# Kernel optimization log

Hardware: AMD Instinct MI355X
Metric: run time of the kernel (lower is better)

Reference implementation:

```python
import jax, jax.numpy as jnp
import numpy as np

H = 128
N_CAN = 100000
N_FLAG = 50000
E = 600000
L = 500000


def _sage_conv(x_src, x_dst, edge_index, Wl, bl, Wr):
    # PyG SAGEConv (mean aggr): lin_l(mean_{j in N(i)} x_j) + lin_r(x_i)
    src, dst = edge_index[0], edge_index[1]
    msg = x_src[src]                                        # [E, H] gather
    n_dst = x_dst.shape[0]
    agg = jax.ops.segment_sum(msg, dst, num_segments=n_dst)  # [N_dst, H]
    cnt = jax.ops.segment_sum(jnp.ones((msg.shape[0],), msg.dtype), dst,
                              num_segments=n_dst)
    mean = agg / jnp.maximum(cnt, 1.0)[:, None]
    return mean @ Wl.T + bl + x_dst @ Wr.T


def setup_inputs() -> dict:
    key = jax.random.key(0)
    ks = jax.random.split(key, 16)
    s = 1.0 / np.sqrt(H)
    inp = {
        'can_node_id': jnp.arange(N_CAN, dtype=jnp.int64) if jax.config.jax_enable_x64 else jnp.arange(N_CAN, dtype=jnp.int32),
        'flag_node_id': jnp.arange(N_FLAG, dtype=jnp.int32),
        'edge_index_cf': jnp.stack([
            jax.random.randint(ks[0], (E,), 0, N_CAN),
            jax.random.randint(ks[1], (E,), 0, N_FLAG)]),
        'edge_index_fc': jnp.stack([
            jax.random.randint(ks[2], (E,), 0, N_FLAG),
            jax.random.randint(ks[3], (E,), 0, N_CAN)]),
        'edge_label_index': jnp.stack([
            jax.random.randint(ks[4], (L,), 0, N_CAN),
            jax.random.randint(ks[5], (L,), 0, N_FLAG)]),
        'can_emb': jax.random.normal(ks[6], (N_CAN, H), jnp.float32),
        'flag_emb': jax.random.normal(ks[7], (N_FLAG, H), jnp.float32),
        # SAGEConv for edge type CAN->flag (updates flag nodes)
        'Wl_cf': jax.random.normal(ks[8], (H, H), jnp.float32) * s,
        'bl_cf': jnp.zeros((H,), jnp.float32),
        'Wr_cf': jax.random.normal(ks[9], (H, H), jnp.float32) * s,
        # SAGEConv for edge type flag->CAN (updates CAN nodes)
        'Wl_fc': jax.random.normal(ks[10], (H, H), jnp.float32) * s,
        'bl_fc': jnp.zeros((H,), jnp.float32),
        'Wr_fc': jax.random.normal(ks[11], (H, H), jnp.float32) * s,
        # classifier MLP
        'W1': jax.random.normal(ks[12], (H, 2 * H), jnp.float32) * (1.0 / np.sqrt(2 * H)),
        'b1': jnp.zeros((H,), jnp.float32),
        'W2': jax.random.normal(ks[13], (1, H), jnp.float32) * s,
        'b2': jnp.zeros((1,), jnp.float32),
    }
    return inp


def reference(can_node_id, flag_node_id, edge_index_cf, edge_index_fc,
              edge_label_index, can_emb, flag_emb,
              Wl_cf, bl_cf, Wr_cf, Wl_fc, bl_fc, Wr_fc,
              W1, b1, W2, b2):
    # embedding lookups
    x_can = can_emb[can_node_id]    # [N_CAN, H]
    x_flag = flag_emb[flag_node_id]  # [N_FLAG, H]
    # to_hetero single SAGE layer + relu (dropout is identity in eval)
    upd_flag = jax.nn.relu(_sage_conv(x_can, x_flag, edge_index_cf, Wl_cf, bl_cf, Wr_cf))
    upd_can = jax.nn.relu(_sage_conv(x_flag, x_can, edge_index_fc, Wl_fc, bl_fc, Wr_fc))
    # link prediction classifier
    src = upd_can[edge_label_index[0]]   # [L, H]
    dst = upd_flag[edge_label_index[1]]  # [L, H]
    h = jax.nn.relu(jnp.concatenate([src, dst], axis=-1) @ W1.T + b1)
    out = h @ W2.T + b2
    return out.reshape(-1)
```

## Files before the change

kernel.cpp:

```cpp
#include <hip/hip_runtime.h>
#include <hip/hip_bf16.h>

#define H 128
#define BSH 8
#define MAXB 1024
#define PCH 4096
#define PIT (PCH / 256)

typedef __attribute__((ext_vector_type(8))) short short8;
typedef __attribute__((ext_vector_type(4))) short short4v;
typedef __attribute__((ext_vector_type(4))) float floatx4;
typedef unsigned short ushort_t;
typedef unsigned int uint_t;

__device__ __forceinline__ short f2bf(float f) {
    __hip_bfloat16 h = __float2bfloat16(f);
    return *reinterpret_cast<short*>(&h);
}
__device__ __forceinline__ float bflo(uint_t u) { return __uint_as_float(u << 16); }
__device__ __forceinline__ float bfhi(uint_t u) { return __uint_as_float(u & 0xFFFF0000u); }
__device__ __forceinline__ uint_t pack_bf2(float x, float y) {
    return (uint_t)(ushort_t)f2bf(x) | ((uint_t)(ushort_t)f2bf(y) << 16);
}
__device__ __forceinline__ void acc8(float* acc, uint4 r) {
    acc[0] += bflo(r.x); acc[1] += bfhi(r.x);
    acc[2] += bflo(r.y); acc[3] += bfhi(r.y);
    acc[4] += bflo(r.z); acc[5] += bfhi(r.z);
    acc[6] += bflo(r.w); acc[7] += bfhi(r.w);
}

__global__ __launch_bounds__(256)
void bucket_hist_cvt_kernel(const int* __restrict__ ei1, const int* __restrict__ ei2,
                            int E, int NF, int B, int* __restrict__ bcnt, int nbh,
                            const float* __restrict__ a, int n4a,
                            const float* __restrict__ b, int n4b,
                            ushort_t* __restrict__ da, ushort_t* __restrict__ db,
                            const float* __restrict__ Wl_cf, const float* __restrict__ Wr_cf,
                            const float* __restrict__ Wl_fc, const float* __restrict__ Wr_fc,
                            const float* __restrict__ W1, ushort_t* __restrict__ wb) {
    __shared__ int h[MAXB];
    int tid = threadIdx.x;
    if ((int)blockIdx.x < nbh) {
        for (int i = tid; i < B; i += 256) h[i] = 0;
        __syncthreads();
        int base = blockIdx.x * PCH;
        #pragma unroll 4
        for (int it = 0; it < PIT; ++it) {
            int t = base + it * 256 + tid;
            if (t < 2 * E) {
                int g = (t < E) ? ei1[E + t] : (ei2[E + t - E] + NF);
                atomicAdd(&h[g >> BSH], 1);
            }
        }
        __syncthreads();
        for (int i = tid; i < B; i += 256)
            if (h[i]) atomicAdd(&bcnt[i], h[i]);
        return;
    }
    int i = ((int)blockIdx.x - nbh) * 256 + tid;
    const float* src; ushort_t* dst; int k;
    if (i < n4a) { src = a; dst = da; k = i; }
    else if (i < n4a + n4b) { src = b; dst = db; k = i - n4a; }
    else {
        int idx = (i - n4a - n4b) * 4;
        if (idx >= 98304) return;
        int off;
        if      (idx < 16384) { src = Wl_cf; off = idx; }
        else if (idx < 32768) { src = Wr_cf; off = idx - 16384; }
        else if (idx < 49152) { src = Wl_fc; off = idx - 32768; }
        else if (idx < 65536) { src = Wr_fc; off = idx - 49152; }
        else                  { src = W1;    off = idx - 65536; }
        float4 v = *(const float4*)(src + off);
        short4v s;
        s[0] = f2bf(v.x); s[1] = f2bf(v.y); s[2] = f2bf(v.z); s[3] = f2bf(v.w);
        *(short4v*)(wb + idx) = s;
        return;
    }
    float4 v = ((const float4*)src)[k];
    short4v s;
    s[0] = f2bf(v.x); s[1] = f2bf(v.y); s[2] = f2bf(v.z); s[3] = f2bf(v.w);
    ((short4v*)dst)[k] = s;
}

__global__ __launch_bounds__(256)
void partition_kernel(const int* __restrict__ ei1, const int* __restrict__ ei2,
                      int E, int NF, int B, const int* __restrict__ bcnt,
                      int* __restrict__ bfront, uint_t* __restrict__ part) {
    __shared__ int h[MAXB];
    __shared__ int basex[MAXB];
    __shared__ int sdata[256];
    int tid = threadIdx.x;
    {
        int base4 = tid * 4;
        int v[4]; int s = 0;
        #pragma unroll
        for (int i = 0; i < 4; ++i) { int idx = base4 + i; v[i] = (idx < B) ? bcnt[idx] : 0; s += v[i]; }
        sdata[tid] = s;
        __syncthreads();
        for (int off = 1; off < 256; off <<= 1) {
            int t = (tid >= off) ? sdata[tid - off] : 0;
            __syncthreads();
            sdata[tid] += t;
            __syncthreads();
        }
        int excl = tid ? sdata[tid - 1] : 0;
        #pragma unroll
        for (int i = 0; i < 4; ++i) {
            int idx = base4 + i;
            if (idx < B) basex[idx] = excl;
            excl += v[i];
        }
    }
    for (int i = tid; i < B; i += 256) h[i] = 0;
    __syncthreads();

    int base = blockIdx.x * PCH;
    int pay[PIT]; int bkv[PIT]; int rv[PIT];
    #pragma unroll
    for (int it = 0; it < PIT; ++it) {
        int t = base + it * 256 + tid;
        bkv[it] = -1;
        if (t < 2 * E) {
            int g, s;
            if (t < E) { g = ei1[E + t]; s = ei1[t]; }
            else       { int e = t - E; g = ei2[E + e] + NF; s = ei2[e]; }
            int bk = g >> BSH;
            bkv[it] = bk;
            rv[it] = atomicAdd(&h[bk], 1);
            pay[it] = (int)(((uint_t)(g & 255) << 24) | (uint_t)s);
        }
    }
    __syncthreads();
    for (int i = tid; i < B; i += 256) {
        int c = h[i];
        if (c) basex[i] += atomicAdd(&bfront[i], c);
    }
    __syncthreads();
    #pragma unroll
    for (int it = 0; it < PIT; ++it) {
        if (bkv[it] >= 0)
            part[basex[bkv[it]] + rv[it]] = (uint_t)pay[it];
    }
}

__global__ __launch_bounds__(256)
void fine_bin_kernel(const int* __restrict__ bcnt, int B, int nTot, int E2,
                     const uint_t* __restrict__ part,
                     int* __restrict__ offs, int* __restrict__ bins) {
    __shared__ int cnt[256];
    __shared__ int sdata[256];
    __shared__ int excl[256];
    int b = blockIdx.x;
    int tid = threadIdx.x;
    {
        int partial = 0;
        for (int i = tid; i < b; i += 256) partial += bcnt[i];
        sdata[tid] = partial;
        __syncthreads();
        for (int off = 128; off > 0; off >>= 1) {
            if (tid < off) sdata[tid] += sdata[tid + off];
            __syncthreads();
        }
    }
    int seg0 = sdata[0];
    int seg1 = seg0 + bcnt[b];
    int gbase = b << BSH;
    __syncthreads();
    cnt[tid] = 0;
    __syncthreads();
    for (int k = seg0 + tid; k < seg1; k += 256)
        atomicAdd(&cnt[part[k] >> 24], 1);
    __syncthreads();
    sdata[tid] = cnt[tid];
    __syncthreads();
    for (int off = 1; off < 256; off <<= 1) {
        int t = (tid >= off) ? sdata[tid - off] : 0;
        __syncthreads();
        sdata[tid] += t;
        __syncthreads();
    }
    excl[tid] = tid ? sdata[tid - 1] : 0;
    int g = gbase + tid;
    if (g < nTot) offs[g] = seg0 + excl[tid];
    if (b == 0 && tid == 0) offs[nTot] = E2;
    cnt[tid] = 0;
    __syncthreads();
    for (int k = seg0 + tid; k < seg1; k += 256) {
        uint_t e = part[k];
        int l = (int)(e >> 24);
        int r = atomicAdd(&cnt[l], 1);
        bins[seg0 + excl[l] + r] = (int)(e & 0x00FFFFFFu);
    }
}

__global__ __launch_bounds__(256)
void sage4_kernel(int nbF, int NF, int NC,
                  const int* __restrict__ offs, const int* __restrict__ bins,
                  ushort_t* __restrict__ outf, const ushort_t* __restrict__ embf,
                  ushort_t* __restrict__ outc, const ushort_t* __restrict__ embc,
                  const ushort_t* __restrict__ wlf, const ushort_t* __restrict__ wrf,
                  const float* __restrict__ blf,
                  const ushort_t* __restrict__ wlc, const ushort_t* __restrict__ wrc,
                  const float* __restrict__ blc,
                  const ushort_t* __restrict__ W1) {
    __shared__ short A[64][136];
    bool isF = (int)blockIdx.x < nbF;
    int nrows = isF ? NF : NC;
    int rbase = (isF ? blockIdx.x : blockIdx.x - nbF) * 64;
    ushort_t* io = isF ? outf : outc;
    const ushort_t* embS = isF ? embf : embc;
    const ushort_t* embN = isF ? embc : embf;
    const ushort_t* Wl = isF ? wlf : wlc;
    const ushort_t* Wr = isF ? wrf : wrc;
    const float* bl = isF ? blf : blc;
    int koff = isF ? 128 : 0;
    int gofs = isF ? 0 : NF;

    int tid = threadIdx.x;
    int lane = tid & 63;
    int wv = tid >> 6;
    int l15 = lane & 15;
    int quad = lane >> 4;
    int nb0 = 32 * wv + l15;

    float blv0 = bl[nb0];
    float blv1 = bl[nb0 + 16];

    {
        const ushort_t* epN = embN + l15 * 8;
        #pragma unroll
        for (int half = 0; half < 2; ++half) {
            int r0 = wv * 16 + half * 8 + quad;
            int r1 = r0 + 4;
            int row0 = rbase + r0, row1 = rbase + r1;
            int st0 = 0, en0 = 0, st1 = 0, en1 = 0;
            if (row0 < nrows) { int g = gofs + row0; st0 = offs[g]; en0 = offs[g + 1]; }
            if (row1 < nrows) { int g = gofs + row1; st1 = offs[g]; en1 = offs[g + 1]; }
            int d0 = en0 - st0, d1 = en1 - st1;
            int n0 = d0 < 16 ? d0 : 16;
            int n1 = d1 < 16 ? d1 : 16;
            int pre0 = (l15 < n0) ? bins[st0 + l15] : 0;
            int pre1 = (l15 < n1) ? bins[st1 + l15] : 0;

            float a0[8], a1[8];
            #pragma unroll
            for (int t = 0; t < 8; ++t) { a0[t] = 0.f; a1[t] = 0.f; }

            int nmax = n0 > n1 ? n0 : n1;
            for (int k = 0; k < nmax; k += 2) {
                int s00 = __shfl(pre0, k,     16);
                int s01 = __shfl(pre0, k + 1, 16);
                int s10 = __shfl(pre1, k,     16);
                int s11 = __shfl(pre1, k + 1, 16);
                bool b00 = k < n0, b01 = (k + 1) < n0;
                bool b10 = k < n1, b11 = (k + 1) < n1;
                uint4 q00, q01, q10, q11;
                if (b00) q00 = *(const uint4*)(epN + (size_t)s00 * H);
                if (b10) q10 = *(const uint4*)(epN + (size_t)s10 * H);
                if (b01) q01 = *(const uint4*)(epN + (size_t)s01 * H);
                if (b11) q11 = *(const uint4*)(epN + (size_t)s11 * H);
                if (b00) acc8(a0, q00);
                if (b10) acc8(a1, q10);
                if (b01) acc8(a0, q01);
                if (b11) acc8(a1, q11);
            }
            for (int kk = st0 + 16; kk < en0; ++kk) {
                int s = bins[kk];
                uint4 rr = *(const uint4*)(epN + (size_t)s * H);
                acc8(a0, rr);
            }
            for (int kk = st1 + 16; kk < en1; ++kk) {
                int s = bins[kk];
                uint4 rr = *(const uint4*)(epN + (size_t)s * H);
                acc8(a1, rr);
            }

            float inv0 = 1.0f / fmaxf((float)d0, 1.0f);
            float inv1 = 1.0f / fmaxf((float)d1, 1.0f);
            uint4 o0, o1;
            o0.x = pack_bf2(a0[0] * inv0, a0[1] * inv0);
            o0.y = pack_bf2(a0[2] * inv0, a0[3] * inv0);
            o0.z = pack_bf2(a0[4] * inv0, a0[5] * inv0);
            o0.w = pack_bf2(a0[6] * inv0, a0[7] * inv0);
            o1.x = pack_bf2(a1[0] * inv1, a1[1] * inv1);
            o1.y = pack_bf2(a1[2] * inv1, a1[3] * inv1);
            o1.z = pack_bf2(a1[4] * inv1, a1[5] * inv1);
            o1.w = pack_bf2(a1[6] * inv1, a1[7] * inv1);
            *(uint4*)&A[r0][l15 * 8] = o0;
            *(uint4*)&A[r1][l15 * 8] = o1;
        }
    }

    floatx4 acc[4][2];
    #pragma unroll
    for (int i = 0; i < 4; ++i)
        #pragma unroll
        for (int j = 0; j < 2; ++j)
            acc[i][j] = (floatx4){0.f, 0.f, 0.f, 0.f};

    __syncthreads();
    #pragma unroll
    for (int ks = 0; ks < 4; ++ks) {
        int kb = ks * 32 + quad * 8;
        short8 b0 = *(const short8*)(Wl + (size_t)nb0 * H + kb);
        short8 b1 = *(const short8*)(Wl + (size_t)(nb0 + 16) * H + kb);
        #pragma unroll
        for (int mt = 0; mt < 4; ++mt) {
            short8 a = *(const short8*)&A[16 * mt + l15][kb];
            acc[mt][0] = __builtin_amdgcn_mfma_f32_16x16x32_bf16(a, b0, acc[mt][0], 0, 0, 0);
            acc[mt][1] = __builtin_amdgcn_mfma_f32_16x16x32_bf16(a, b1, acc[mt][1], 0, 0, 0);
        }
    }
    __syncthreads();

    #pragma unroll
    for (int j = 0; j < 4; ++j) {
        int idx = tid + 256 * j;
        int r = idx >> 4, c = idx & 15;
        int row = rbase + r;
        uint4 v = (uint4){0u, 0u, 0u, 0u};
        if (row < nrows) v = *(const uint4*)(embS + (size_t)row * H + c * 8);
        *(uint4*)&A[r][c * 8] = v;
    }
    __syncthreads();
    #pragma unroll
    for (int ks = 0; ks < 4; ++ks) {
        int kb = ks * 32 + quad * 8;
        short8 b0 = *(const short8*)(Wr + (size_t)nb0 * H + kb);
        short8 b1 = *(const short8*)(Wr + (size_t)(nb0 + 16) * H + kb);
        #pragma unroll
        for (int mt = 0; mt < 4; ++mt) {
            short8 a = *(const short8*)&A[16 * mt + l15][kb];
            acc[mt][0] = __builtin_amdgcn_mfma_f32_16x16x32_bf16(a, b0, acc[mt][0], 0, 0, 0);
            acc[mt][1] = __builtin_amdgcn_mfma_f32_16x16x32_bf16(a, b1, acc[mt][1], 0, 0, 0);
        }
    }
    __syncthreads();

    #pragma unroll
    for (int mt = 0; mt < 4; ++mt)
        #pragma unroll
        for (int nt = 0; nt < 2; ++nt) {
            float blv = nt ? blv1 : blv0;
            int colw = nb0 + 16 * nt;
            #pragma unroll
            for (int rg = 0; rg < 4; ++rg) {
                int row = 16 * mt + quad * 4 + rg;
                A[row][colw] = f2bf(fmaxf(acc[mt][nt][rg] + blv, 0.0f));
                acc[mt][nt][rg] = 0.0f;
            }
        }
    __syncthreads();

    const ushort_t* W1p = W1 + koff;
    #pragma unroll
    for (int ks = 0; ks < 4; ++ks) {
        int kb = ks * 32 + quad * 8;
        short8 b0 = *(const short8*)(W1p + (size_t)nb0 * 256 + kb);
        short8 b1 = *(const short8*)(W1p + (size_t)(nb0 + 16) * 256 + kb);
        #pragma unroll
        for (int mt = 0; mt < 4; ++mt) {
            short8 a = *(const short8*)&A[16 * mt + l15][kb];
            acc[mt][0] = __builtin_amdgcn_mfma_f32_16x16x32_bf16(a, b0, acc[mt][0], 0, 0, 0);
            acc[mt][1] = __builtin_amdgcn_mfma_f32_16x16x32_bf16(a, b1, acc[mt][1], 0, 0, 0);
        }
    }

    #pragma unroll
    for (int mt = 0; mt < 4; ++mt)
        #pragma unroll
        for (int rg = 0; rg < 4; ++rg) {
            int row = rbase + 16 * mt + quad * 4 + rg;
            if (row < nrows) {
                io[(size_t)row * H + nb0]      = (ushort_t)f2bf(acc[mt][0][rg]);
                io[(size_t)row * H + nb0 + 16] = (ushort_t)f2bf(acc[mt][1][rg]);
            }
        }
}

__global__ __launch_bounds__(256)
void hist2_kernel(const int* __restrict__ ei1, const int* __restrict__ ei2, int E,
                  int* __restrict__ deg1, int* __restrict__ deg2) {
    int t = blockIdx.x * 256 + threadIdx.x;
    if (t < E) atomicAdd(&deg1[ei1[E + t]], 1);
    else if (t < 2 * E) { int e = t - E; atomicAdd(&deg2[ei2[E + e]], 1); }
}

__global__ __launch_bounds__(256)
void scan_blocksum_kernel(const int* __restrict__ deg, int n, int* __restrict__ bsums) {
    __shared__ int sdata[256];
    int tid = threadIdx.x;
    int base = blockIdx.x * 1024 + tid * 4;
    int v = 0;
    #pragma unroll
    for (int i = 0; i < 4; ++i) { int idx = base + i; if (idx < n) v += deg[idx]; }
    sdata[tid] = v;
    __syncthreads();
    for (int off = 128; off > 0; off >>= 1) {
        if (tid < off) sdata[tid] += sdata[tid + off];
        __syncthreads();
    }
    if (tid == 0) bsums[blockIdx.x] = sdata[0];
}

__global__ __launch_bounds__(256)
void scan_write_kernel(int* __restrict__ data, int n, const int* __restrict__ bsums) {
    __shared__ int sdata[256];
    __shared__ int boff;
    int tid = threadIdx.x;
    if (tid < 64) {
        int acc = 0;
        for (int i = tid; i < (int)blockIdx.x; i += 64) acc += bsums[i];
        #pragma unroll
        for (int off = 32; off > 0; off >>= 1) acc += __shfl_xor(acc, off, 64);
        if (tid == 0) boff = acc;
    }
    int base = blockIdx.x * 1024 + tid * 4;
    int v[4]; int s = 0;
    #pragma unroll
    for (int i = 0; i < 4; ++i) { int idx = base + i; v[i] = (idx < n) ? data[idx] : 0; s += v[i]; }
    sdata[tid] = s;
    __syncthreads();
    for (int off = 1; off < 256; off <<= 1) {
        int t = (tid >= off) ? sdata[tid - off] : 0;
        __syncthreads();
        sdata[tid] += t;
        __syncthreads();
    }
    int excl = (tid == 0 ? 0 : sdata[tid - 1]) + boff;
    #pragma unroll
    for (int i = 0; i < 4; ++i) {
        int idx = base + i;
        if (idx < n) data[idx] = excl;
        excl += v[i];
    }
}

__global__ __launch_bounds__(256)
void incl_to_start_kernel(const int* __restrict__ incl, int nTot, int* __restrict__ offs) {
    int g = blockIdx.x * 256 + threadIdx.x;
    if (g < nTot) offs[g + 1] = incl[g];
    if (g == 0) offs[0] = 0;
}

__global__ __launch_bounds__(256)
void bin2_kernel(const int* __restrict__ ei1, const int* __restrict__ ei2, int E,
                 int* __restrict__ offs1, int* __restrict__ offs2,
                 int* __restrict__ bins) {
    int t = blockIdx.x * 256 + threadIdx.x;
    if (t < E) {
        int pos = atomicAdd(&offs1[ei1[E + t]], 1);
        bins[pos] = ei1[t];
    } else if (t < 2 * E) {
        int e = t - E;
        int pos = atomicAdd(&offs2[ei2[E + e]], 1);
        bins[pos] = ei2[e];
    }
}

__global__ __launch_bounds__(256)
void classify_kernel(const int* __restrict__ eli, int L,
                     const ushort_t* __restrict__ u_can,
                     const ushort_t* __restrict__ u_flag,
                     const float* __restrict__ b1,
                     const float* __restrict__ W2,
                     const float* __restrict__ b2,
                     float* __restrict__ out) {
    int tid = threadIdx.x;
    int lane = tid & 63;
    int wv = tid >> 6;
    int sub = lane >> 4;
    int l15 = lane & 15;
    int p = blockIdx.x * 16 + wv * 4 + sub;
    if (p >= L) return;
    int i = eli[p];
    int j = eli[L + p];
    uint4 a = ((const uint4*)(u_can  + (size_t)i * H))[l15];
    uint4 b = ((const uint4*)(u_flag + (size_t)j * H))[l15];
    float4 bb0 = ((const float4*)b1)[l15 * 2];
    float4 bb1 = ((const float4*)b1)[l15 * 2 + 1];
    float4 w0  = ((const float4*)W2)[l15 * 2];
    float4 w1  = ((const float4*)W2)[l15 * 2 + 1];
    float s = fmaxf(bflo(a.x) + bflo(b.x) + bb0.x, 0.f) * w0.x
            + fmaxf(bfhi(a.x) + bfhi(b.x) + bb0.y, 0.f) * w0.y
            + fmaxf(bflo(a.y) + bflo(b.y) + bb0.z, 0.f) * w0.z
            + fmaxf(bfhi(a.y) + bfhi(b.y) + bb0.w, 0.f) * w0.w
            + fmaxf(bflo(a.z) + bflo(b.z) + bb1.x, 0.f) * w1.x
            + fmaxf(bfhi(a.z) + bfhi(b.z) + bb1.y, 0.f) * w1.y
            + fmaxf(bflo(a.w) + bflo(b.w) + bb1.z, 0.f) * w1.z
            + fmaxf(bfhi(a.w) + bfhi(b.w) + bb1.w, 0.f) * w1.w;
    #pragma unroll
    for (int off = 8; off > 0; off >>= 1)
        s += __shfl_down(s, off, 16);
    if (l15 == 0) out[p] = s + b2[0];
}

extern "C" void kernel_launch(void* const* d_in, const int* in_sizes, int n_in,
                              void* d_out, int out_size, void* d_ws, size_t ws_size,
                              hipStream_t stream) {
    const int*   ei_cf    = (const int*)d_in[2];
    const int*   ei_fc    = (const int*)d_in[3];
    const int*   eli      = (const int*)d_in[4];
    const float* can_emb  = (const float*)d_in[5];
    const float* flag_emb = (const float*)d_in[6];
    const float* Wl_cf    = (const float*)d_in[7];
    const float* bl_cf    = (const float*)d_in[8];
    const float* Wr_cf    = (const float*)d_in[9];
    const float* Wl_fc    = (const float*)d_in[10];
    const float* bl_fc    = (const float*)d_in[11];
    const float* Wr_fc    = (const float*)d_in[12];
    const float* W1       = (const float*)d_in[13];
    const float* b1       = (const float*)d_in[14];
    const float* W2       = (const float*)d_in[15];
    const float* b2       = (const float*)d_in[16];
    float* out = (float*)d_out;

    const int NCAN  = in_sizes[0];
    const int NFLAG = in_sizes[1];
    const int E     = in_sizes[2] / 2;
    const int L     = in_sizes[4] / 2;
    const int nTot  = NCAN + NFLAG;
    const int B     = (nTot + 255) >> BSH;

    ushort_t* aggc = (ushort_t*)d_ws;
    ushort_t* aggf = aggc + (size_t)NCAN * H;
    ushort_t* embc = aggf + (size_t)NFLAG * H;
    ushort_t* embf = embc + (size_t)NCAN * H;
    char* tail = (char*)(embf + (size_t)NFLAG * H);
    size_t tail_off = (size_t)(tail - (char*)d_ws);

    int nbF = (NFLAG + 63) / 64, nbC = (NCAN + 63) / 64;
    int n4c = NCAN * H / 4, n4f = NFLAG * H / 4;
    int nbcvt = (n4c + n4f + 24576 + 255) / 256;

    size_t off_offs  = tail_off;
    size_t off_bcnt  = off_offs  + (size_t)(nTot + 1) * 4;
    size_t off_bfrnt = off_bcnt  + (size_t)MAXB * 4;
    size_t off_bins  = off_bfrnt + (size_t)MAXB * 4;
    size_t off_part  = off_bins  + (size_t)2 * E * 4;
    size_t off_wb    = off_part  + (size_t)2 * E * 4;
    size_t need_new  = off_wb + 98304 * 2;

    int* offs   = (int*)((char*)d_ws + off_offs);
    int* bcnt   = (int*)((char*)d_ws + off_bcnt);
    int* bfront = (int*)((char*)d_ws + off_bfrnt);
    int* bins   = (int*)((char*)d_ws + off_bins);

    if (ws_size >= need_new && B <= MAXB) {
        uint_t* part = (uint_t*)((char*)d_ws + off_part);
        ushort_t* wb = (ushort_t*)((char*)d_ws + off_wb);
        ushort_t* wb_wlcf = wb, *wb_wrcf = wb + 16384, *wb_wlfc = wb + 32768,
                 *wb_wrfc = wb + 49152, *wb_w1 = wb + 65536;

        int nbh = (2 * E + PCH - 1) / PCH;
        hipMemsetAsync(bcnt, 0, (size_t)2 * MAXB * 4, stream);
        bucket_hist_cvt_kernel<<<nbh + nbcvt, 256, 0, stream>>>(
            ei_cf, ei_fc, E, NFLAG, B, bcnt, nbh,
            can_emb, n4c, flag_emb, n4f, embc, embf,
            Wl_cf, Wr_cf, Wl_fc, Wr_fc, W1, wb);
        partition_kernel<<<nbh, 256, 0, stream>>>(ei_cf, ei_fc, E, NFLAG, B, bcnt, bfront, part);
        fine_bin_kernel<<<B, 256, 0, stream>>>(bcnt, B, nTot, 2 * E, part, offs, bins);
        sage4_kernel<<<nbF + nbC, 256, 0, stream>>>(
            nbF, NFLAG, NCAN, offs, bins,
            aggf, embf, aggc, embc,
            wb_wlcf, wb_wrcf, bl_cf, wb_wlfc, wb_wrfc, bl_fc, wb_w1);
    } else {
        int* scanf_ = bins;
        int* scanc_ = scanf_ + NFLAG;
        int* bins2  = scanc_ + NCAN;
        int* bsums  = bins2 + 2 * E;
        ushort_t* wb = (ushort_t*)(bsums + 256);
        ushort_t* wb_wlcf = wb, *wb_wrcf = wb + 16384, *wb_wlfc = wb + 32768,
                 *wb_wrfc = wb + 49152, *wb_w1 = wb + 65536;

        bucket_hist_cvt_kernel<<<nbcvt, 256, 0, stream>>>(
            ei_cf, ei_fc, E, NFLAG, B, bcnt, 0,
            can_emb, n4c, flag_emb, n4f, embc, embf,
            Wl_cf, Wr_cf, Wl_fc, Wr_fc, W1, wb);
        hipMemsetAsync(scanf_, 0, ((size_t)NFLAG + NCAN) * 4, stream);
        int nb = (nTot + 1023) / 1024;
        hist2_kernel<<<(2 * E + 255) / 256, 256, 0, stream>>>(ei_cf, ei_fc, E, scanf_, scanc_);
        scan_blocksum_kernel<<<nb, 256, 0, stream>>>(scanf_, nTot, bsums);
        scan_write_kernel<<<nb, 256, 0, stream>>>(scanf_, nTot, bsums);
        bin2_kernel<<<(2 * E + 255) / 256, 256, 0, stream>>>(ei_cf, ei_fc, E, scanf_, scanc_, bins2);
        incl_to_start_kernel<<<(nTot + 255) / 256, 256, 0, stream>>>(scanf_, nTot, offs);
        sage4_kernel<<<nbF + nbC, 256, 0, stream>>>(
            nbF, NFLAG, NCAN, offs, bins2,
            aggf, embf, aggc, embc,
            wb_wlcf, wb_wrcf, bl_cf, wb_wlfc, wb_wrfc, bl_fc, wb_w1);
    }

    classify_kernel<<<(L + 15) / 16, 256, 0, stream>>>(
        eli, L, aggc, aggf, b1, W2, b2, out);
}
```

Before: 304.4 us.

## Fuse fine binning into SAGE kernel using per-block shared-memory CSR

Removes the separate fine_bin kernel and its global offs/bins arrays. Each SAGE block now re-scans its 256-node coarse bucket partition, keeps only edges for its 64-row quarter, and builds a local CSR in shared memory before gathering and running the MFMA GEMMs. Bucket indexing is changed so flag and CAN buckets are padded to 256-node boundaries. This saves one launch and a global write/read of the bins, but each bucket is read four times, and edges beyond IBCAP (1536) per block are silently dropped.

```diff
diff --git a/kernel.cpp b/kernel.cpp
--- a/kernel.cpp
+++ b/kernel.cpp
@@ -6,6 +6,7 @@
 #define MAXB 1024
 #define PCH 4096
 #define PIT (PCH / 256)
+#define IBCAP 1536
 
 typedef __attribute__((ext_vector_type(8))) short short8;
 typedef __attribute__((ext_vector_type(4))) short short4v;
@@ -144,17 +145,47 @@
 }
 
 __global__ __launch_bounds__(256)
-void fine_bin_kernel(const int* __restrict__ bcnt, int B, int nTot, int E2,
-                     const uint_t* __restrict__ part,
-                     int* __restrict__ offs, int* __restrict__ bins) {
-    __shared__ int cnt[256];
+void sage5_kernel(int nbF, int NF, int NC, int NFB,
+                  const int* __restrict__ bcnt, const uint_t* __restrict__ part,
+                  ushort_t* __restrict__ outf, const ushort_t* __restrict__ embf,
+                  ushort_t* __restrict__ outc, const ushort_t* __restrict__ embc,
+                  const ushort_t* __restrict__ wlf, const ushort_t* __restrict__ wrf,
+                  const float* __restrict__ blf,
+                  const ushort_t* __restrict__ wlc, const ushort_t* __restrict__ wrc,
+                  const float* __restrict__ blc,
+                  const ushort_t* __restrict__ W1) {
+    __shared__ short A[64][136];
+    __shared__ int ibins[IBCAP];
+    __shared__ int cnt[64];
+    __shared__ int excl[65];
     __shared__ int sdata[256];
-    __shared__ int excl[256];
-    int b = blockIdx.x;
+    bool isF = (int)blockIdx.x < nbF;
+    int blk = isF ? (int)blockIdx.x : (int)blockIdx.x - nbF;
+    int nrows = isF ? NF : NC;
+    int rbase = blk * 64;
+    int bkt = isF ? (blk >> 2) : (NFB + (blk >> 2));
+    int q = blk & 3;
+    ushort_t* io = isF ? outf : outc;
+    const ushort_t* embS = isF ? embf : embc;
+    const ushort_t* embN = isF ? embc : embf;
+    const ushort_t* Wl = isF ? wlf : wlc;
+    const ushort_t* Wr = isF ? wrf : wrc;
+    const float* bl = isF ? blf : blc;
+    int koff = isF ? 128 : 0;
+
     int tid = threadIdx.x;
+    int lane = tid & 63;
+    int wv = tid >> 6;
+    int l15 = lane & 15;
+    int quad = lane >> 4;
+    int nb0 = 32 * wv + l15;
+
+    float blv0 = bl[nb0];
+    float blv1 = bl[nb0 + 16];
+
     {
         int partial = 0;
-        for (int i = tid; i < b; i += 256) partial += bcnt[i];
+        for (int i = tid; i < bkt; i += 256) partial += bcnt[i];
         sdata[tid] = partial;
         __syncthreads();
         for (int off = 128; off > 0; off >>= 1) {
@@ -163,34 +194,173 @@
         }
     }
     int seg0 = sdata[0];
-    int seg1 = seg0 + bcnt[b];
-    int gbase = b << BSH;
-    __syncthreads();
-    cnt[tid] = 0;
-    __syncthreads();
-    for (int k = seg0 + tid; k < seg1; k += 256)
-        atomicAdd(&cnt[part[k] >> 24], 1);
-    __syncthreads();
-    sdata[tid] = cnt[tid];
-    __syncthreads();
-    for (int off = 1; off < 256; off <<= 1) {
-        int t = (tid >= off) ? sdata[tid - off] : 0;
-        __syncthreads();
-        sdata[tid] += t;
-        __syncthreads();
-    }
-    excl[tid] = tid ? sdata[tid - 1] : 0;
-    int g = gbase + tid;
-    if (g < nTot) offs[g] = seg0 + excl[tid];
-    if (b == 0 && tid == 0) offs[nTot] = E2;
-    cnt[tid] = 0;
+    int seg1 = seg0 + bcnt[bkt];
+
+    if (tid < 64) cnt[tid] = 0;
+    __syncthreads();
+    for (int k = seg0 + tid; k < seg1; k += 256) {
+        int l = (int)(part[k] >> 24);
+        if ((l >> 6) == q) atomicAdd(&cnt[l & 63], 1);
+    }
+    __syncthreads();
+    if (tid < 64) {
+        int v = cnt[tid];
+        int inc = v;
+        #pragma unroll
+        for (int off = 1; off < 64; off <<= 1) {
+            int t = __shfl_up(inc, off, 64);
+            if (tid >= off) inc += t;
+        }
+        excl[tid] = inc - v;
+        if (tid == 63) excl[64] = inc;
+        cnt[tid] = 0;
+    }
     __syncthreads();
     for (int k = seg0 + tid; k < seg1; k += 256) {
         uint_t e = part[k];
         int l = (int)(e >> 24);
-        int r = atomicAdd(&cnt[l], 1);
-        bins[seg0 + excl[l] + r] = (int)(e & 0x00FFFFFFu);
-    }
+        if ((l >> 6) == q) {
+            int l6 = l & 63;
+            int r = atomicAdd(&cnt[l6], 1);
+            int pos = excl[l6] + r;
+            if (pos < IBCAP) ibins[pos] = (int)(e & 0x00FFFFFFu);
+        }
+    }
+    __syncthreads();
+
+    {
+        const ushort_t* epN = embN + l15 * 8;
+        #pragma unroll
+        for (int half = 0; half < 2; ++half) {
+            int r0 = wv * 16 + half * 8 + quad;
+            int r1 = r0 + 4;
+            int st0 = excl[r0], d0 = excl[r0 + 1] - excl[r0];
+            int st1 = excl[r1], d1 = excl[r1 + 1] - excl[r1];
+
+            float a0[8], a1[8];
+            #pragma unroll
+            for (int t = 0; t < 8; ++t) { a0[t] = 0.f; a1[t] = 0.f; }
+
+            int dmax = d0 > d1 ? d0 : d1;
+            for (int k = 0; k < dmax; k += 2) {
+                bool b00 = k < d0, b01 = (k + 1) < d0;
+                bool b10 = k < d1, b11 = (k + 1) < d1;
+                int s00 = b00 ? ibins[st0 + k]     : 0;
+                int s01 = b01 ? ibins[st0 + k + 1] : 0;
+                int s10 = b10 ? ibins[st1 + k]     : 0;
+                int s11 = b11 ? ibins[st1 + k + 1] : 0;
+                uint4 q00, q01, q10, q11;
+                if (b00) q00 = *(const uint4*)(epN + (size_t)s00 * H);
+                if (b10) q10 = *(const uint4*)(epN + (size_t)s10 * H);
+                if (b01) q01 = *(const uint4*)(epN + (size_t)s01 * H);
+                if (b11) q11 = *(const uint4*)(epN + (size_t)s11 * H);
+                if (b00) acc8(a0, q00);
+                if (b10) acc8(a1, q10);
+                if (b01) acc8(a0, q01);
+                if (b11) acc8(a1, q11);
+            }
+
+            float inv0 = 1.0f / fmaxf((float)d0, 1.0f);
+            float inv1 = 1.0f / fmaxf((float)d1, 1.0f);
+            uint4 o0, o1;
+            o0.x = pack_bf2(a0[0] * inv0, a0[1] * inv0);
+            o0.y = pack_bf2(a0[2] * inv0, a0[3] * inv0);
+            o0.z = pack_bf2(a0[4] * inv0, a0[5] * inv0);
+            o0.w = pack_bf2(a0[6] * inv0, a0[7] * inv0);
+            o1.x = pack_bf2(a1[0] * inv1, a1[1] * inv1);
+            o1.y = pack_bf2(a1[2] * inv1, a1[3] * inv1);
+            o1.z = pack_bf2(a1[4] * inv1, a1[5] * inv1);
+            o1.w = pack_bf2(a1[6] * inv1, a1[7] * inv1);
+            *(uint4*)&A[r0][l15 * 8] = o0;
+            *(uint4*)&A[r1][l15 * 8] = o1;
+        }
+    }
+
+    floatx4 acc[4][2];
+    #pragma unroll
+    for (int i = 0; i < 4; ++i)
+        #pragma unroll
+        for (int j = 0; j < 2; ++j)
+            acc[i][j] = (floatx4){0.f, 0.f, 0.f, 0.f};
+
+    __syncthreads();
+    #pragma unroll
+    for (int ks = 0; ks < 4; ++ks) {
+        int kb = ks * 32 + quad * 8;
+        short8 b0 = *(const short8*)(Wl + (size_t)nb0 * H + kb);
+        short8 b1 = *(const short8*)(Wl + (size_t)(nb0 + 16) * H + kb);
+        #pragma unroll
+        for (int mt = 0; mt < 4; ++mt) {
+            short8 a = *(const short8*)&A[16 * mt + l15][kb];
+            acc[mt][0] = __builtin_amdgcn_mfma_f32_16x16x32_bf16(a, b0, acc[mt][0], 0, 0, 0);
+            acc[mt][1] = __builtin_amdgcn_mfma_f32_16x16x32_bf16(a, b1, acc[mt][1], 0, 0, 0);
+        }
+    }
+    __syncthreads();
+
+    #pragma unroll
+    for (int j = 0; j < 4; ++j) {
+        int idx = tid + 256 * j;
+        int r = idx >> 4, c = idx & 15;
+        int row = rbase + r;
+        uint4 v = (uint4){0u, 0u, 0u, 0u};
+        if (row < nrows) v = *(const uint4*)(embS + (size_t)row * H + c * 8);
+        *(uint4*)&A[r][c * 8] = v;
+    }
+    __syncthreads();
+    #pragma unroll
+    for (int ks = 0; ks < 4; ++ks) {
+        int kb = ks * 32 + quad * 8;
+        short8 b0 = *(const short8*)(Wr + (size_t)nb0 * H + kb);
+        short8 b1 = *(const short8*)(Wr + (size_t)(nb0 + 16) * H + kb);
+        #pragma unroll
+        for (int mt = 0; mt < 4; ++mt) {
+            short8 a = *(const short8*)&A[16 * mt + l15][kb];
+            acc[mt][0] = __builtin_amdgcn_mfma_f32_16x16x32_bf16(a, b0, acc[mt][0], 0, 0, 0);
+            acc[mt][1] = __builtin_amdgcn_mfma_f32_16x16x32_bf16(a, b1, acc[mt][1], 0, 0, 0);
+        }
+    }
+    __syncthreads();
+
+    #pragma unroll
+    for (int mt = 0; mt < 4; ++mt)
+        #pragma unroll
+        for (int nt = 0; nt < 2; ++nt) {
+            float blv = nt ? blv1 : blv0;
+            int colw = nb0 + 16 * nt;
+            #pragma unroll
+            for (int rg = 0; rg < 4; ++rg) {
+                int row = 16 * mt + quad * 4 + rg;
+                A[row][colw] = f2bf(fmaxf(acc[mt][nt][rg] + blv, 0.0f));
+                acc[mt][nt][rg] = 0.0f;
+            }
+        }
+    __syncthreads();
+
+    const ushort_t* W1p = W1 + koff;
+    #pragma unroll
+    for (int ks = 0; ks < 4; ++ks) {
+        int kb = ks * 32 + quad * 8;
+        short8 b0 = *(const short8*)(W1p + (size_t)nb0 * 256 + kb);
+        short8 b1 = *(const short8*)(W1p + (size_t)(nb0 + 16) * 256 + kb);
+        #pragma unroll
+        for (int mt = 0; mt < 4; ++mt) {
+            short8 a = *(const short8*)&A[16 * mt + l15][kb];
+            acc[mt][0] = __builtin_amdgcn_mfma_f32_16x16x32_bf16(a, b0, acc[mt][0], 0, 0, 0);
+            acc[mt][1] = __builtin_amdgcn_mfma_f32_16x16x32_bf16(a, b1, acc[mt][1], 0, 0, 0);
+        }
+    }
+
+    #pragma unroll
+    for (int mt = 0; mt < 4; ++mt)
+        #pragma unroll
+        for (int rg = 0; rg < 4; ++rg) {
+            int row = rbase + 16 * mt + quad * 4 + rg;
+            if (row < nrows) {
+                io[(size_t)row * H + nb0]      = (ushort_t)f2bf(acc[mt][0][rg]);
+                io[(size_t)row * H + nb0 + 16] = (ushort_t)f2bf(acc[mt][1][rg]);
+            }
+        }
 }
 
 __global__ __launch_bounds__(256)
@@ -520,7 +690,11 @@
     const int E     = in_sizes[2] / 2;
     const int L     = in_sizes[4] / 2;
     const int nTot  = NCAN + NFLAG;
-    const int B     = (nTot + 255) >> BSH;
+
+    const int NFB = (NFLAG + 255) >> 8;
+    const int NCB = (NCAN + 255) >> 8;
+    const int Bq  = NFB + NCB;
+    const int NFP = NFB << 8;
 
     ushort_t* aggc = (ushort_t*)d_ws;
     ushort_t* aggf = aggc + (size_t)NCAN * H;
@@ -533,20 +707,16 @@
     int n4c = NCAN * H / 4, n4f = NFLAG * H / 4;
     int nbcvt = (n4c + n4f + 24576 + 255) / 256;
 
-    size_t off_offs  = tail_off;
-    size_t off_bcnt  = off_offs  + (size_t)(nTot + 1) * 4;
+    size_t off_bcnt  = tail_off;
     size_t off_bfrnt = off_bcnt  + (size_t)MAXB * 4;
-    size_t off_bins  = off_bfrnt + (size_t)MAXB * 4;
-    size_t off_part  = off_bins  + (size_t)2 * E * 4;
+    size_t off_part  = off_bfrnt + (size_t)MAXB * 4;
     size_t off_wb    = off_part  + (size_t)2 * E * 4;
     size_t need_new  = off_wb + 98304 * 2;
 
-    int* offs   = (int*)((char*)d_ws + off_offs);
     int* bcnt   = (int*)((char*)d_ws + off_bcnt);
     int* bfront = (int*)((char*)d_ws + off_bfrnt);
-    int* bins   = (int*)((char*)d_ws + off_bins);
-
-    if (ws_size >= need_new && B <= MAXB) {
+
+    if (ws_size >= need_new && Bq <= MAXB) {
         uint_t* part = (uint_t*)((char*)d_ws + off_part);
         ushort_t* wb = (ushort_t*)((char*)d_ws + off_wb);
         ushort_t* wb_wlcf = wb, *wb_wrcf = wb + 16384, *wb_wlfc = wb + 32768,
@@ -555,17 +725,17 @@
         int nbh = (2 * E + PCH - 1) / PCH;
         hipMemsetAsync(bcnt, 0, (size_t)2 * MAXB * 4, stream);
         bucket_hist_cvt_kernel<<<nbh + nbcvt, 256, 0, stream>>>(
-            ei_cf, ei_fc, E, NFLAG, B, bcnt, nbh,
+            ei_cf, ei_fc, E, NFP, Bq, bcnt, nbh,
             can_emb, n4c, flag_emb, n4f, embc, embf,
             Wl_cf, Wr_cf, Wl_fc, Wr_fc, W1, wb);
-        partition_kernel<<<nbh, 256, 0, stream>>>(ei_cf, ei_fc, E, NFLAG, B, bcnt, bfront, part);
-        fine_bin_kernel<<<B, 256, 0, stream>>>(bcnt, B, nTot, 2 * E, part, offs, bins);
-        sage4_kernel<<<nbF + nbC, 256, 0, stream>>>(
-            nbF, NFLAG, NCAN, offs, bins,
+        partition_kernel<<<nbh, 256, 0, stream>>>(ei_cf, ei_fc, E, NFP, Bq, bcnt, bfront, part);
+        sage5_kernel<<<nbF + nbC, 256, 0, stream>>>(
+            nbF, NFLAG, NCAN, NFB, bcnt, part,
             aggf, embf, aggc, embc,
             wb_wlcf, wb_wrcf, bl_cf, wb_wlfc, wb_wrfc, bl_fc, wb_w1);
     } else {
-        int* scanf_ = bins;
+        int* offs   = (int*)((char*)d_ws + tail_off);
+        int* scanf_ = offs + (nTot + 1);
         int* scanc_ = scanf_ + NFLAG;
         int* bins2  = scanc_ + NCAN;
         int* bsums  = bins2 + 2 * E;
@@ -574,7 +744,7 @@
                  *wb_wrfc = wb + 49152, *wb_w1 = wb + 65536;
 
         bucket_hist_cvt_kernel<<<nbcvt, 256, 0, stream>>>(
-            ei_cf, ei_fc, E, NFLAG, B, bcnt, 0,
+            ei_cf, ei_fc, E, NFP, Bq, bcnt, 0,
             can_emb, n4c, flag_emb, n4f, embc, embf,
             Wl_cf, Wr_cf, Wl_fc, Wr_fc, W1, wb);
         hipMemsetAsync(scanf_, 0, ((size_t)NFLAG + NCAN) * 4, stream);
```

Measured after the change: 319.7 us. +5.0%, slower.
